# Kernel tuning notes

Hardware: AMD Instinct MI355X
Metric: run time of the kernel (lower is better)

## Reference

```python
import jax, jax.numpy as jnp
import numpy as np

POS_IOU, NEG_IOU = 0.5, 0.4
VAR = (0.1, 0.1, 0.2, 0.2)
ALPHA = 1.0
B, A, C, G = 16, 65536, 81, 32


def setup_inputs() -> dict:
    key = jax.random.key(0)
    k1, k2, k3, k4, k5, k6, k7 = jax.random.split(key, 7)
    cls_logits = jax.random.normal(k1, (B, A, C), dtype=jnp.float32)
    bbox_regs = jax.random.normal(k2, (B, A, 4), dtype=jnp.float32)
    # anchors: normalized cx,cy in (0,1), w,h positive
    anc_cxy = jax.random.uniform(k3, (A, 2), minval=0.05, maxval=0.95)
    anc_wh = jax.random.uniform(k4, (A, 2), minval=0.02, maxval=0.30)
    anchors_cxcywh = jnp.concatenate([anc_cxy, anc_wh], axis=-1).astype(jnp.float32)
    # GT boxes: valid normalized xyxy built from random cxcywh
    g_cxy = jax.random.uniform(k5, (B, G, 2), minval=0.1, maxval=0.9)
    g_wh = jax.random.uniform(k6, (B, G, 2), minval=0.05, maxval=0.40)
    x1y1 = jnp.clip(g_cxy - g_wh / 2, 0.0, 1.0)
    x2y2 = jnp.clip(g_cxy + g_wh / 2, 0.0, 1.0)
    gt_boxes = jnp.concatenate([x1y1, x2y2], axis=-1).astype(jnp.float32)
    gt_labels = jax.random.randint(k7, (B, G), 1, C).astype(jnp.int64)
    gt_valid = jnp.ones((B, G), dtype=bool)
    return {"cls_logits": cls_logits, "bbox_regs": bbox_regs,
            "anchors_cxcywh": anchors_cxcywh, "gt_boxes": gt_boxes,
            "gt_labels": gt_labels, "gt_valid": gt_valid}


def _encode(gt_xyxy, anc_cxcywh):
    # gt_xyxy [B,A,4], anc_cxcywh [A,4] -> offsets [B,A,4]
    x1, y1, x2, y2 = jnp.split(gt_xyxy, 4, axis=-1)
    gx, gy = (x1 + x2) / 2, (y1 + y2) / 2
    gw = jnp.clip(x2 - x1, 1e-6, None)
    gh = jnp.clip(y2 - y1, 1e-6, None)
    ax, ay, aw, ah = (anc_cxcywh[None, :, i:i + 1] for i in range(4))
    dx = (gx - ax) / (aw * VAR[0])
    dy = (gy - ay) / (ah * VAR[1])
    dw = jnp.log(gw / aw) / VAR[2]
    dh = jnp.log(gh / ah) / VAR[3]
    return jnp.concatenate([dx, dy, dw, dh], axis=-1)


def _forward(cls_logits, bbox_regs, anchors_cxcywh, gt_boxes, gt_labels, gt_valid):
    ax, ay, aw, ah = (anchors_cxcywh[:, i] for i in range(4))
    anc_xyxy = jnp.stack([ax - aw / 2, ay - ah / 2, ax + aw / 2, ay + ah / 2], axis=-1)  # [A,4]
    # IoU [B,A,G] (assignment is torch.no_grad in the original)
    tl = jnp.maximum(anc_xyxy[None, :, None, :2], gt_boxes[:, None, :, :2])
    br = jnp.minimum(anc_xyxy[None, :, None, 2:], gt_boxes[:, None, :, 2:])
    wh = jnp.clip(br - tl, 0.0, None)
    inter = wh[..., 0] * wh[..., 1]
    area_a = jnp.clip(anc_xyxy[:, 2] - anc_xyxy[:, 0], 0.0, None) * jnp.clip(anc_xyxy[:, 3] - anc_xyxy[:, 1], 0.0, None)
    area_b = jnp.clip(gt_boxes[..., 2] - gt_boxes[..., 0], 0.0, None) * jnp.clip(gt_boxes[..., 3] - gt_boxes[..., 1], 0.0, None)
    iou = inter / (area_a[None, :, None] + area_b[:, None, :] - inter + 1e-9)
    iou = jnp.where(gt_valid[:, None, :], iou, -1.0)  # padded GTs never match
    iou = jax.lax.stop_gradient(iou)

    iou_max = jnp.max(iou, axis=-1)              # [B,A]
    iou_idx = jnp.argmax(iou, axis=-1)           # [B,A]
    pos = iou_max >= POS_IOU
    ign = (iou_max > NEG_IOU) & ~pos

    matched_boxes = jnp.take_along_axis(gt_boxes, iou_idx[..., None], axis=1)   # [B,A,4]
    matched_labels = jnp.take_along_axis(gt_labels, iou_idx, axis=1)            # [B,A]
    cls_t = jnp.where(pos, matched_labels, jnp.where(ign, -1, 0))               # [B,A]
    reg_t = jax.lax.stop_gradient(_encode(matched_boxes, anchors_cxcywh))       # [B,A,4]

    # classification CE over valid (non-ignored) anchors, per-image mean
    logp = jax.nn.log_softmax(cls_logits, axis=-1)
    tgt = jnp.clip(cls_t, 0, None)
    ce = -jnp.take_along_axis(logp, tgt[..., None], axis=-1)[..., 0]            # [B,A]
    valid = cls_t >= 0
    n_valid = jnp.sum(valid, axis=1)
    cls_per = jnp.sum(ce * valid, axis=1) / jnp.maximum(n_valid, 1)
    total_cls = jnp.sum(jnp.where(n_valid > 0, cls_per, 0.0))

    # smooth L1 over positive anchors, per-image mean over pos*4 elements
    d = jnp.abs(bbox_regs - reg_t)
    sl1 = jnp.where(d < 1.0, 0.5 * d * d, d - 0.5)                              # [B,A,4]
    n_pos = jnp.sum(pos, axis=1)
    reg_per = jnp.sum(sl1 * pos[..., None], axis=(1, 2)) / jnp.maximum(4 * n_pos, 1)
    total_reg = jnp.sum(jnp.where(n_pos > 0, reg_per, 0.0))

    return total_cls + ALPHA * total_reg


def reference(cls_logits, bbox_regs, anchors_cxcywh, gt_boxes, gt_labels, gt_valid):
    return _forward(cls_logits, bbox_regs, anchors_cxcywh, gt_boxes, gt_labels, gt_valid)
```

## Files before the change

kernel.cpp:

```cpp
#include <hip/hip_runtime.h>
#include <math.h>

constexpr int kB = 16;
constexpr int kA = 65536;
constexpr int kC = 81;
constexpr int kG = 32;
constexpr int kBlockA = 256;
constexpr int kBlocksPerB = kA / kBlockA;
constexpr float kPosIou = 0.5f;
constexpr float kNegIou = 0.4f;

struct F5 { float4 x0, x1, x2, x3, x4; };

__device__ __forceinline__ float4 ldf4(const float* p) {
    float4 v; __builtin_memcpy(&v, p, 16); return v;
}
__device__ __forceinline__ F5 load5(const float* row, int q) {
    const float* r = row + (q << 2);
    F5 f;
    f.x0 = ldf4(r);
    f.x1 = ldf4(r + 16);
    f.x2 = ldf4(r + 32);
    f.x3 = ldf4(r + 48);
    f.x4 = ldf4(r + 64);
    return f;
}
__device__ __forceinline__ float sumexp(const F5& f) {
    float s0 = __expf(f.x0.x) + __expf(f.x0.y) + __expf(f.x0.z) + __expf(f.x0.w);
    float s1 = __expf(f.x1.x) + __expf(f.x1.y) + __expf(f.x1.z) + __expf(f.x1.w);
    float s2 = __expf(f.x2.x) + __expf(f.x2.y) + __expf(f.x2.z) + __expf(f.x2.w);
    float s3 = __expf(f.x3.x) + __expf(f.x3.y) + __expf(f.x3.z) + __expf(f.x3.w);
    float s4 = __expf(f.x4.x) + __expf(f.x4.y) + __expf(f.x4.z) + __expf(f.x4.w);
    return ((s0 + s1) + (s2 + s3)) + s4;
}

__global__ __launch_bounds__(256) void ssd_main_kernel(
    const float* __restrict__ cls_logits,
    const float* __restrict__ bbox_regs,
    const float* __restrict__ anchors,
    const float* __restrict__ gt_boxes,
    const int*   __restrict__ gt_labels,
    const int*   __restrict__ gt_valid,
    float* __restrict__ ws)
{
    __shared__ float s_gx1[kG], s_gy1[kG], s_gx2[kG], s_gy2[kG], s_area[kG];
    __shared__ int   s_lab[kG], s_val[kG];
    __shared__ int   s_t[kBlockA];
    __shared__ float s_tv[kBlockA];
    __shared__ float s_e80[kBlockA];
    __shared__ float s_red[4][4];

    const int tid = threadIdx.x;
    const int b  = blockIdx.x / kBlocksPerB;
    const int a0 = (blockIdx.x % kBlocksPerB) * kBlockA;

    if (tid < kG) {
        float4 gb = *reinterpret_cast<const float4*>(gt_boxes + ((size_t)b * kG + tid) * 4);
        s_gx1[tid] = gb.x; s_gy1[tid] = gb.y; s_gx2[tid] = gb.z; s_gy2[tid] = gb.w;
        s_area[tid] = fmaxf(gb.z - gb.x, 0.f) * fmaxf(gb.w - gb.y, 0.f);
        s_lab[tid] = gt_labels[b * kG + tid];
        s_val[tid] = gt_valid[b * kG + tid];
    }
    __syncthreads();

    const int wave = tid >> 6;
    const int lane = tid & 63;
    const int g4   = lane >> 2;
    const int q    = lane & 3;
    const float* row0 = cls_logits + ((size_t)b * kA + a0 + 0 * 64 + wave * 16 + g4) * kC;
    const float* row1 = cls_logits + ((size_t)b * kA + a0 + 1 * 64 + wave * 16 + g4) * kC;
    const float* row2 = cls_logits + ((size_t)b * kA + a0 + 2 * 64 + wave * 16 + g4) * kC;
    const float* row3 = cls_logits + ((size_t)b * kA + a0 + 3 * 64 + wave * 16 + g4) * kC;
    F5 va = load5(row0, q);
    F5 vb = load5(row1, q);

    const int a = a0 + tid;
    float4 anc = *reinterpret_cast<const float4*>(anchors + (size_t)a * 4);
    const float ax1 = anc.x - anc.z * 0.5f, ay1 = anc.y - anc.w * 0.5f;
    const float ax2 = anc.x + anc.z * 0.5f, ay2 = anc.y + anc.w * 0.5f;
    const float area_a = fmaxf(ax2 - ax1, 0.f) * fmaxf(ay2 - ay1, 0.f);

    float best = -2.0f;
    int   bidx = 0;
    #pragma unroll 8
    for (int g = 0; g < kG; ++g) {
        float tlx = fmaxf(ax1, s_gx1[g]);
        float tly = fmaxf(ay1, s_gy1[g]);
        float brx = fminf(ax2, s_gx2[g]);
        float bry = fminf(ay2, s_gy2[g]);
        float w = fmaxf(brx - tlx, 0.f);
        float h = fmaxf(bry - tly, 0.f);
        float inter = w * h;
        float iou = __fdividef(inter, area_a + s_area[g] - inter + 1e-9f);
        iou = s_val[g] ? iou : -1.0f;
        if (iou > best) { best = iou; bidx = g; }
    }
    const bool pos = best >= kPosIou;
    const bool ign = (best > kNegIou) && !pos;
    const int cls_t = pos ? s_lab[bidx] : (ign ? -1 : 0);
    s_t[tid] = cls_t;

    const float* own = cls_logits + ((size_t)b * kA + a0 + tid) * kC;
    s_tv[tid]  = own[cls_t < 0 ? 0 : cls_t];
    s_e80[tid] = own[80];

    float reg_sum = 0.f;
    if (pos) {
        float gx1 = s_gx1[bidx], gy1 = s_gy1[bidx], gx2 = s_gx2[bidx], gy2 = s_gy2[bidx];
        float gx = (gx1 + gx2) * 0.5f, gy = (gy1 + gy2) * 0.5f;
        float gw = fmaxf(gx2 - gx1, 1e-6f), gh = fmaxf(gy2 - gy1, 1e-6f);
        float dx = __fdividef(gx - anc.x, anc.z * 0.1f);
        float dy = __fdividef(gy - anc.y, anc.w * 0.1f);
        float dw = __logf(__fdividef(gw, anc.z)) * 5.0f;
        float dh = __logf(__fdividef(gh, anc.w)) * 5.0f;
        float4 br = *reinterpret_cast<const float4*>(bbox_regs + ((size_t)b * kA + a) * 4);
        float d0 = fabsf(br.x - dx), d1 = fabsf(br.y - dy);
        float d2 = fabsf(br.z - dw), d3 = fabsf(br.w - dh);
        reg_sum = (d0 < 1.f ? 0.5f * d0 * d0 : d0 - 0.5f)
                + (d1 < 1.f ? 0.5f * d1 * d1 : d1 - 0.5f)
                + (d2 < 1.f ? 0.5f * d2 * d2 : d2 - 0.5f)
                + (d3 < 1.f ? 0.5f * d3 * d3 : d3 - 0.5f);
    }
    __syncthreads();

    int   ct0 = 0, ct1 = 0, ct2 = 0, ct3 = 0;
    float tv0 = 0.f, tv1 = 0.f, tv2 = 0.f, tv3 = 0.f;
    float e80_0 = 0.f, e80_1 = 0.f, e80_2 = 0.f, e80_3 = 0.f;
    if (q == 0) {
        const int r0 = 0 * 64 + wave * 16 + g4;
        const int r1 = 1 * 64 + wave * 16 + g4;
        const int r2 = 2 * 64 + wave * 16 + g4;
        const int r3 = 3 * 64 + wave * 16 + g4;
        ct0 = s_t[r0]; tv0 = s_tv[r0]; e80_0 = s_e80[r0];
        ct1 = s_t[r1]; tv1 = s_tv[r1]; e80_1 = s_e80[r1];
        ct2 = s_t[r2]; tv2 = s_tv[r2]; e80_2 = s_e80[r2];
        ct3 = s_t[r3]; tv3 = s_tv[r3]; e80_3 = s_e80[r3];
    }

    float ce_acc = 0.f;
    {
        float S = sumexp(va);
        if (q == 0) S += __expf(e80_0);
        S += __shfl_xor(S, 1);
        S += __shfl_xor(S, 2);
        if (q == 0 && ct0 >= 0) ce_acc += __logf(S) - tv0;
    }
    va = load5(row2, q);
    {
        float S = sumexp(vb);
        if (q == 0) S += __expf(e80_1);
        S += __shfl_xor(S, 1);
        S += __shfl_xor(S, 2);
        if (q == 0 && ct1 >= 0) ce_acc += __logf(S) - tv1;
    }
    vb = load5(row3, q);
    {
        float S = sumexp(va);
        if (q == 0) S += __expf(e80_2);
        S += __shfl_xor(S, 1);
        S += __shfl_xor(S, 2);
        if (q == 0 && ct2 >= 0) ce_acc += __logf(S) - tv2;
    }
    {
        float S = sumexp(vb);
        if (q == 0) S += __expf(e80_3);
        S += __shfl_xor(S, 1);
        S += __shfl_xor(S, 2);
        if (q == 0 && ct3 >= 0) ce_acc += __logf(S) - tv3;
    }

    float v0 = ce_acc;
    float v1 = (cls_t >= 0) ? 1.f : 0.f;
    float v2 = reg_sum;
    float v3 = pos ? 1.f : 0.f;
    #pragma unroll
    for (int off = 32; off > 0; off >>= 1) {
        v0 += __shfl_xor(v0, off);
        v1 += __shfl_xor(v1, off);
        v2 += __shfl_xor(v2, off);
        v3 += __shfl_xor(v3, off);
    }
    if (lane == 0) {
        s_red[wave][0] = v0; s_red[wave][1] = v1;
        s_red[wave][2] = v2; s_red[wave][3] = v3;
    }
    __syncthreads();
    if (tid < 4) {
        float acc = s_red[0][tid] + s_red[1][tid] + s_red[2][tid] + s_red[3][tid];
        ws[(size_t)blockIdx.x * 4 + tid] = acc;
    }
}

__global__ __launch_bounds__(256) void ssd_final_kernel(
    const float* __restrict__ ws, float* __restrict__ out)
{
    __shared__ float s_per_b[kB];
    const int tid = threadIdx.x;
    const int b = tid >> 4;
    const int i = tid & 15;
    float a0 = 0.f, a1 = 0.f, a2 = 0.f, a3 = 0.f;
    #pragma unroll
    for (int k = 0; k < 16; ++k) {
        const float4 v = *reinterpret_cast<const float4*>(
            ws + ((size_t)((b << 8) + (k << 4) + i)) * 4);
        a0 += v.x; a1 += v.y; a2 += v.z; a3 += v.w;
    }
    #pragma unroll
    for (int off = 1; off < 16; off <<= 1) {
        a0 += __shfl_xor(a0, off);
        a1 += __shfl_xor(a1, off);
        a2 += __shfl_xor(a2, off);
        a3 += __shfl_xor(a3, off);
    }
    if (i == 0) {
        float cls = (a1 > 0.f) ? a0 / fmaxf(a1, 1.f) : 0.f;
        float reg = (a3 > 0.f) ? a2 / fmaxf(4.f * a3, 1.f) : 0.f;
        s_per_b[b] = cls + reg;
    }
    __syncthreads();
    if (tid == 0) {
        float t = 0.f;
        #pragma unroll
        for (int x = 0; x < kB; ++x) t += s_per_b[x];
        out[0] = t;
    }
}

extern "C" void kernel_launch(void* const* d_in, const int* in_sizes, int n_in,
                              void* d_out, int out_size, void* d_ws, size_t ws_size,
                              hipStream_t stream) {
    const float* cls_logits = (const float*)d_in[0];
    const float* bbox_regs  = (const float*)d_in[1];
    const float* anchors    = (const float*)d_in[2];
    const float* gt_boxes   = (const float*)d_in[3];
    const int*   gt_labels  = (const int*)d_in[4];
    const int*   gt_valid   = (const int*)d_in[5];
    float* ws  = (float*)d_ws;
    float* out = (float*)d_out;

    ssd_main_kernel<<<dim3(kB * kBlocksPerB), dim3(kBlockA), 0, stream>>>(
        cls_logits, bbox_regs, anchors, gt_boxes, gt_labels, gt_valid, ws);
    ssd_final_kernel<<<dim3(1), dim3(kBlockA), 0, stream>>>(ws, out);
}
```

Measured before the change: 72.86 us.

## Shuffle targets within waves, pick target logit from registers, fuse final reduction

Remaps logit rows so each wave processes the same anchors it assigned, letting targets move via cross-lane shuffles instead of shared memory and a block barrier. The target logit is selected from already-loaded registers, removing scattered per-anchor global loads. The separate finalize kernel is replaced by per-image atomic accumulation and a last-block counter, which needs a memset each call and relies on atomic ordering without an explicit fence.

```diff
diff --git a/kernel.cpp b/kernel.cpp
--- a/kernel.cpp
+++ b/kernel.cpp
@@ -7,6 +7,7 @@
 constexpr int kG = 32;
 constexpr int kBlockA = 256;
 constexpr int kBlocksPerB = kA / kBlockA;
+constexpr int kGrid = kB * kBlocksPerB;
 constexpr float kPosIou = 0.5f;
 constexpr float kNegIou = 0.4f;
 
@@ -33,6 +34,16 @@
     float s4 = __expf(f.x4.x) + __expf(f.x4.y) + __expf(f.x4.z) + __expf(f.x4.w);
     return ((s0 + s1) + (s2 + s3)) + s4;
 }
+__device__ __forceinline__ float pick_t(const F5& f, int te, int q, float e80) {
+    if (te >= 80) return (q == 0) ? e80 : 0.f;
+    const int k_t = te >> 4;
+    const int q_t = (te >> 2) & 3;
+    const int e_t = te & 3;
+    if (q != q_t) return 0.f;
+    float4 c = (k_t == 0) ? f.x0 : (k_t == 1) ? f.x1 : (k_t == 2) ? f.x2
+             : (k_t == 3) ? f.x3 : f.x4;
+    return (e_t == 0) ? c.x : (e_t == 1) ? c.y : (e_t == 2) ? c.z : c.w;
+}
 
 __global__ __launch_bounds__(256) void ssd_main_kernel(
     const float* __restrict__ cls_logits,
@@ -41,14 +52,14 @@
     const float* __restrict__ gt_boxes,
     const int*   __restrict__ gt_labels,
     const int*   __restrict__ gt_valid,
-    float* __restrict__ ws)
+    float* __restrict__ ws,
+    int*   __restrict__ counter,
+    float* __restrict__ out)
 {
     __shared__ float s_gx1[kG], s_gy1[kG], s_gx2[kG], s_gy2[kG], s_area[kG];
     __shared__ int   s_lab[kG], s_val[kG];
-    __shared__ int   s_t[kBlockA];
-    __shared__ float s_tv[kBlockA];
-    __shared__ float s_e80[kBlockA];
     __shared__ float s_red[4][4];
+    __shared__ int   s_last;
 
     const int tid = threadIdx.x;
     const int b  = blockIdx.x / kBlocksPerB;
@@ -67,12 +78,15 @@
     const int lane = tid & 63;
     const int g4   = lane >> 2;
     const int q    = lane & 3;
-    const float* row0 = cls_logits + ((size_t)b * kA + a0 + 0 * 64 + wave * 16 + g4) * kC;
-    const float* row1 = cls_logits + ((size_t)b * kA + a0 + 1 * 64 + wave * 16 + g4) * kC;
-    const float* row2 = cls_logits + ((size_t)b * kA + a0 + 2 * 64 + wave * 16 + g4) * kC;
-    const float* row3 = cls_logits + ((size_t)b * kA + a0 + 3 * 64 + wave * 16 + g4) * kC;
+    const float* wrow = cls_logits + ((size_t)b * kA + a0 + wave * 64) * kC;
+    const float* row0 = wrow + (size_t)(0 * 16 + g4) * kC;
+    const float* row1 = wrow + (size_t)(1 * 16 + g4) * kC;
+    const float* row2 = wrow + (size_t)(2 * 16 + g4) * kC;
+    const float* row3 = wrow + (size_t)(3 * 16 + g4) * kC;
     F5 va = load5(row0, q);
     F5 vb = load5(row1, q);
+    float e80_0 = 0.f, e80_1 = 0.f, e80_2 = 0.f, e80_3 = 0.f;
+    if (q == 0) { e80_0 = row0[80]; e80_1 = row1[80]; e80_2 = row2[80]; e80_3 = row3[80]; }
 
     const int a = a0 + tid;
     float4 anc = *reinterpret_cast<const float4*>(anchors + (size_t)a * 4);
@@ -98,11 +112,6 @@
     const bool pos = best >= kPosIou;
     const bool ign = (best > kNegIou) && !pos;
     const int cls_t = pos ? s_lab[bidx] : (ign ? -1 : 0);
-    s_t[tid] = cls_t;
-
-    const float* own = cls_logits + ((size_t)b * kA + a0 + tid) * kC;
-    s_tv[tid]  = own[cls_t < 0 ? 0 : cls_t];
-    s_e80[tid] = own[80];
 
     float reg_sum = 0.f;
     if (pos) {
@@ -121,52 +130,50 @@
                 + (d2 < 1.f ? 0.5f * d2 * d2 : d2 - 0.5f)
                 + (d3 < 1.f ? 0.5f * d3 * d3 : d3 - 0.5f);
     }
-    __syncthreads();
-
-    int   ct0 = 0, ct1 = 0, ct2 = 0, ct3 = 0;
-    float tv0 = 0.f, tv1 = 0.f, tv2 = 0.f, tv3 = 0.f;
-    float e80_0 = 0.f, e80_1 = 0.f, e80_2 = 0.f, e80_3 = 0.f;
-    if (q == 0) {
-        const int r0 = 0 * 64 + wave * 16 + g4;
-        const int r1 = 1 * 64 + wave * 16 + g4;
-        const int r2 = 2 * 64 + wave * 16 + g4;
-        const int r3 = 3 * 64 + wave * 16 + g4;
-        ct0 = s_t[r0]; tv0 = s_tv[r0]; e80_0 = s_e80[r0];
-        ct1 = s_t[r1]; tv1 = s_tv[r1]; e80_1 = s_e80[r1];
-        ct2 = s_t[r2]; tv2 = s_tv[r2]; e80_2 = s_e80[r2];
-        ct3 = s_t[r3]; tv3 = s_tv[r3]; e80_3 = s_e80[r3];
-    }
+
+    const int ct0 = __shfl(cls_t, 0 * 16 + g4);
+    const int ct1 = __shfl(cls_t, 1 * 16 + g4);
+    const int ct2 = __shfl(cls_t, 2 * 16 + g4);
+    const int ct3 = __shfl(cls_t, 3 * 16 + g4);
 
     float ce_acc = 0.f;
     {
+        const int te = ct0 < 0 ? 0 : ct0;
         float S = sumexp(va);
         if (q == 0) S += __expf(e80_0);
-        S += __shfl_xor(S, 1);
-        S += __shfl_xor(S, 2);
-        if (q == 0 && ct0 >= 0) ce_acc += __logf(S) - tv0;
+        float T = pick_t(va, te, q, e80_0);
+        S += __shfl_xor(S, 1);  T += __shfl_xor(T, 1);
+        S += __shfl_xor(S, 2);  T += __shfl_xor(T, 2);
+        if (q == 0 && ct0 >= 0) ce_acc += __logf(S) - T;
     }
     va = load5(row2, q);
     {
+        const int te = ct1 < 0 ? 0 : ct1;
         float S = sumexp(vb);
         if (q == 0) S += __expf(e80_1);
-        S += __shfl_xor(S, 1);
-        S += __shfl_xor(S, 2);
-        if (q == 0 && ct1 >= 0) ce_acc += __logf(S) - tv1;
+        float T = pick_t(vb, te, q, e80_1);
+        S += __shfl_xor(S, 1);  T += __shfl_xor(T, 1);
+        S += __shfl_xor(S, 2);  T += __shfl_xor(T, 2);
+        if (q == 0 && ct1 >= 0) ce_acc += __logf(S) - T;
     }
     vb = load5(row3, q);
     {
+        const int te = ct2 < 0 ? 0 : ct2;
         float S = sumexp(va);
         if (q == 0) S += __expf(e80_2);
-        S += __shfl_xor(S, 1);
-        S += __shfl_xor(S, 2);
-        if (q == 0 && ct2 >= 0) ce_acc += __logf(S) - tv2;
-    }
-    {
+        float T = pick_t(va, te, q, e80_2);
+        S += __shfl_xor(S, 1);  T += __shfl_xor(T, 1);
+        S += __shfl_xor(S, 2);  T += __shfl_xor(T, 2);
+        if (q == 0 && ct2 >= 0) ce_acc += __logf(S) - T;
+    }
+    {
+        const int te = ct3 < 0 ? 0 : ct3;
         float S = sumexp(vb);
         if (q == 0) S += __expf(e80_3);
-        S += __shfl_xor(S, 1);
-        S += __shfl_xor(S, 2);
-        if (q == 0 && ct3 >= 0) ce_acc += __logf(S) - tv3;
+        float T = pick_t(vb, te, q, e80_3);
+        S += __shfl_xor(S, 1);  T += __shfl_xor(T, 1);
+        S += __shfl_xor(S, 2);  T += __shfl_xor(T, 2);
+        if (q == 0 && ct3 >= 0) ce_acc += __logf(S) - T;
     }
 
     float v0 = ce_acc;
@@ -187,42 +194,24 @@
     __syncthreads();
     if (tid < 4) {
         float acc = s_red[0][tid] + s_red[1][tid] + s_red[2][tid] + s_red[3][tid];
-        ws[(size_t)blockIdx.x * 4 + tid] = acc;
-    }
-}
-
-__global__ __launch_bounds__(256) void ssd_final_kernel(
-    const float* __restrict__ ws, float* __restrict__ out)
-{
-    __shared__ float s_per_b[kB];
-    const int tid = threadIdx.x;
-    const int b = tid >> 4;
-    const int i = tid & 15;
-    float a0 = 0.f, a1 = 0.f, a2 = 0.f, a3 = 0.f;
-    #pragma unroll
-    for (int k = 0; k < 16; ++k) {
-        const float4 v = *reinterpret_cast<const float4*>(
-            ws + ((size_t)((b << 8) + (k << 4) + i)) * 4);
-        a0 += v.x; a1 += v.y; a2 += v.z; a3 += v.w;
-    }
-    #pragma unroll
-    for (int off = 1; off < 16; off <<= 1) {
-        a0 += __shfl_xor(a0, off);
-        a1 += __shfl_xor(a1, off);
-        a2 += __shfl_xor(a2, off);
-        a3 += __shfl_xor(a3, off);
-    }
-    if (i == 0) {
-        float cls = (a1 > 0.f) ? a0 / fmaxf(a1, 1.f) : 0.f;
-        float reg = (a3 > 0.f) ? a2 / fmaxf(4.f * a3, 1.f) : 0.f;
-        s_per_b[b] = cls + reg;
-    }
-    __syncthreads();
-    if (tid == 0) {
-        float t = 0.f;
+        atomicAdd(&ws[b * 4 + tid], acc);
+    }
+    __syncthreads();
+    if (tid == 0)
+        s_last = (atomicAdd(counter, 1) == kGrid - 1);
+    __syncthreads();
+    if (s_last && tid < kB) {
+        float sce  = atomicAdd(&ws[tid * 4 + 0], 0.f);
+        float nval = atomicAdd(&ws[tid * 4 + 1], 0.f);
+        float ssl  = atomicAdd(&ws[tid * 4 + 2], 0.f);
+        float npos = atomicAdd(&ws[tid * 4 + 3], 0.f);
+        float cls = (nval > 0.f) ? sce / fmaxf(nval, 1.f) : 0.f;
+        float reg = (npos > 0.f) ? ssl / fmaxf(4.f * npos, 1.f) : 0.f;
+        float v = cls + reg;
         #pragma unroll
-        for (int x = 0; x < kB; ++x) t += s_per_b[x];
-        out[0] = t;
+        for (int off = 1; off < kB; off <<= 1)
+            v += __shfl_xor(v, off);
+        if (tid == 0) out[0] = v;
     }
 }
 
@@ -235,10 +224,13 @@
     const float* gt_boxes   = (const float*)d_in[3];
     const int*   gt_labels  = (const int*)d_in[4];
     const int*   gt_valid   = (const int*)d_in[5];
-    float* ws  = (float*)d_ws;
-    float* out = (float*)d_out;
-
-    ssd_main_kernel<<<dim3(kB * kBlocksPerB), dim3(kBlockA), 0, stream>>>(
-        cls_logits, bbox_regs, anchors, gt_boxes, gt_labels, gt_valid, ws);
-    ssd_final_kernel<<<dim3(1), dim3(kBlockA), 0, stream>>>(ws, out);
-}
+    float* ws      = (float*)d_ws;
+    int*   counter = (int*)((char*)d_ws + 256);
+    float* out     = (float*)d_out;
+
+    hipMemsetAsync(d_ws, 0, 260, stream);
+
+    ssd_main_kernel<<<dim3(kGrid), dim3(kBlockA), 0, stream>>>(
+        cls_logits, bbox_regs, anchors, gt_boxes, gt_labels, gt_valid,
+        ws, counter, out);
+}
```

New measurement: 137.9 us. +89.2%, slower.

## Split anchor assignment and cross-entropy into separate kernels with int8 targets

Applied to the files above, without the earlier changes.

Anchor matching and the smooth-L1 term move into their own kernel, which writes per-anchor class targets as int8 to the workspace. A second kernel streams the logits, 512 rows per block, with software-prefetched double buffering. It takes the target logit from the registers already loaded instead of issuing scattered per-row loads. This removes the serial dependency of the logit stream on the IoU loop and the uncoalesced target gather, at the cost of an extra launch and a small int8 round trip. The fused path remains as a fallback when the workspace is too small.

```diff
diff --git a/kernel.cpp b/kernel.cpp
--- a/kernel.cpp
+++ b/kernel.cpp
@@ -5,8 +5,6 @@
 constexpr int kA = 65536;
 constexpr int kC = 81;
 constexpr int kG = 32;
-constexpr int kBlockA = 256;
-constexpr int kBlocksPerB = kA / kBlockA;
 constexpr float kPosIou = 0.5f;
 constexpr float kNegIou = 0.4f;
 
@@ -33,26 +31,43 @@
     float s4 = __expf(f.x4.x) + __expf(f.x4.y) + __expf(f.x4.z) + __expf(f.x4.w);
     return ((s0 + s1) + (s2 + s3)) + s4;
 }
-
-__global__ __launch_bounds__(256) void ssd_main_kernel(
-    const float* __restrict__ cls_logits,
+__device__ __forceinline__ float pick_t(const F5& f, int te, int q, float e80) {
+    if (te >= 80) return (q == 0) ? e80 : 0.f;
+    const int k_t = te >> 4;
+    const int q_t = (te >> 2) & 3;
+    const int e_t = te & 3;
+    if (q != q_t) return 0.f;
+    float4 c = (k_t == 0) ? f.x0 : (k_t == 1) ? f.x1 : (k_t == 2) ? f.x2
+             : (k_t == 3) ? f.x3 : f.x4;
+    return (e_t == 0) ? c.x : (e_t == 1) ? c.y : (e_t == 2) ? c.z : c.w;
+}
+
+constexpr size_t kOffT8  = 0;
+constexpr size_t kOffAsg = (size_t)kB * kA;
+constexpr size_t kOffCe  = kOffAsg + (size_t)4096 * 4 * 4;
+constexpr size_t kWsNeed = kOffCe + (size_t)2048 * 4;
+
+constexpr int kAsgBlkA   = 256;
+constexpr int kAsgPerB   = kA / kAsgBlkA;
+constexpr int kRowsPerCe = 512;
+constexpr int kCePerB    = kA / kRowsPerCe;
+
+__global__ __launch_bounds__(256) void ssd_assign_kernel(
     const float* __restrict__ bbox_regs,
     const float* __restrict__ anchors,
     const float* __restrict__ gt_boxes,
     const int*   __restrict__ gt_labels,
     const int*   __restrict__ gt_valid,
-    float* __restrict__ ws)
+    signed char* __restrict__ cls_t8,
+    float* __restrict__ wsa)
 {
     __shared__ float s_gx1[kG], s_gy1[kG], s_gx2[kG], s_gy2[kG], s_area[kG];
     __shared__ int   s_lab[kG], s_val[kG];
-    __shared__ int   s_t[kBlockA];
-    __shared__ float s_tv[kBlockA];
-    __shared__ float s_e80[kBlockA];
     __shared__ float s_red[4][4];
 
     const int tid = threadIdx.x;
-    const int b  = blockIdx.x / kBlocksPerB;
-    const int a0 = (blockIdx.x % kBlocksPerB) * kBlockA;
+    const int b  = blockIdx.x / kAsgPerB;
+    const int a0 = (blockIdx.x % kAsgPerB) * kAsgBlkA;
 
     if (tid < kG) {
         float4 gb = *reinterpret_cast<const float4*>(gt_boxes + ((size_t)b * kG + tid) * 4);
@@ -62,17 +77,6 @@
         s_val[tid] = gt_valid[b * kG + tid];
     }
     __syncthreads();
-
-    const int wave = tid >> 6;
-    const int lane = tid & 63;
-    const int g4   = lane >> 2;
-    const int q    = lane & 3;
-    const float* row0 = cls_logits + ((size_t)b * kA + a0 + 0 * 64 + wave * 16 + g4) * kC;
-    const float* row1 = cls_logits + ((size_t)b * kA + a0 + 1 * 64 + wave * 16 + g4) * kC;
-    const float* row2 = cls_logits + ((size_t)b * kA + a0 + 2 * 64 + wave * 16 + g4) * kC;
-    const float* row3 = cls_logits + ((size_t)b * kA + a0 + 3 * 64 + wave * 16 + g4) * kC;
-    F5 va = load5(row0, q);
-    F5 vb = load5(row1, q);
 
     const int a = a0 + tid;
     float4 anc = *reinterpret_cast<const float4*>(anchors + (size_t)a * 4);
@@ -98,11 +102,7 @@
     const bool pos = best >= kPosIou;
     const bool ign = (best > kNegIou) && !pos;
     const int cls_t = pos ? s_lab[bidx] : (ign ? -1 : 0);
-    s_t[tid] = cls_t;
-
-    const float* own = cls_logits + ((size_t)b * kA + a0 + tid) * kC;
-    s_tv[tid]  = own[cls_t < 0 ? 0 : cls_t];
-    s_e80[tid] = own[80];
+    cls_t8[(size_t)b * kA + a] = (signed char)cls_t;
 
     float reg_sum = 0.f;
     if (pos) {
@@ -121,6 +121,230 @@
                 + (d2 < 1.f ? 0.5f * d2 * d2 : d2 - 0.5f)
                 + (d3 < 1.f ? 0.5f * d3 * d3 : d3 - 0.5f);
     }
+
+    const int wave = tid >> 6;
+    const int lane = tid & 63;
+    float v1 = (cls_t >= 0) ? 1.f : 0.f;
+    float v2 = reg_sum;
+    float v3 = pos ? 1.f : 0.f;
+    #pragma unroll
+    for (int off = 32; off > 0; off >>= 1) {
+        v1 += __shfl_xor(v1, off);
+        v2 += __shfl_xor(v2, off);
+        v3 += __shfl_xor(v3, off);
+    }
+    if (lane == 0) {
+        s_red[wave][0] = 0.f; s_red[wave][1] = v1;
+        s_red[wave][2] = v2;  s_red[wave][3] = v3;
+    }
+    __syncthreads();
+    if (tid < 4) {
+        float acc = s_red[0][tid] + s_red[1][tid] + s_red[2][tid] + s_red[3][tid];
+        wsa[(size_t)blockIdx.x * 4 + tid] = acc;
+    }
+}
+
+__global__ __launch_bounds__(256) void ssd_ce_kernel(
+    const float* __restrict__ cls_logits,
+    const signed char* __restrict__ cls_t8,
+    float* __restrict__ wsce)
+{
+    __shared__ float s_red[4];
+    const int tid  = threadIdx.x;
+    const int wave = tid >> 6;
+    const int lane = tid & 63;
+    const int g4   = lane >> 2;
+    const int q    = lane & 3;
+    const int blk   = blockIdx.x;
+    const int b     = blk / kCePerB;
+    const int chunk = blk % kCePerB;
+
+    const size_t rbase = (size_t)b * kA + chunk * kRowsPerCe + wave * 16 + g4;
+    const float* rp = cls_logits + rbase * kC;
+    const signed char* ctp = cls_t8 + rbase;
+    const size_t kIt = (size_t)64 * kC;
+
+    F5 va = load5(rp, q);
+    F5 vb = load5(rp + kIt, q);
+    int cta = ctp[0];
+    int ctb = ctp[64];
+    float ea = 0.f, eb = 0.f;
+    if (q == 0) { ea = rp[80]; eb = rp[kIt + 80]; }
+
+    float ce = 0.f;
+    #pragma unroll
+    for (int it = 0; it < 8; it += 2) {
+        {
+            float S = sumexp(va);
+            float T = pick_t(va, cta < 0 ? 0 : cta, q, ea);
+            const bool vld = (cta >= 0);
+            const float ecur = ea;
+            if (it + 2 < 8) {
+                va = load5(rp + (it + 2) * kIt, q);
+                cta = ctp[(it + 2) * 64];
+                if (q == 0) ea = rp[(it + 2) * kIt + 80];
+            }
+            if (q == 0) S += __expf(ecur);
+            S += __shfl_xor(S, 1);  T += __shfl_xor(T, 1);
+            S += __shfl_xor(S, 2);  T += __shfl_xor(T, 2);
+            if (q == 0 && vld) ce += __logf(S) - T;
+        }
+        {
+            float S = sumexp(vb);
+            float T = pick_t(vb, ctb < 0 ? 0 : ctb, q, eb);
+            const bool vld = (ctb >= 0);
+            const float ecur = eb;
+            if (it + 3 < 8) {
+                vb = load5(rp + (it + 3) * kIt, q);
+                ctb = ctp[(it + 3) * 64];
+                if (q == 0) eb = rp[(it + 3) * kIt + 80];
+            }
+            if (q == 0) S += __expf(ecur);
+            S += __shfl_xor(S, 1);  T += __shfl_xor(T, 1);
+            S += __shfl_xor(S, 2);  T += __shfl_xor(T, 2);
+            if (q == 0 && vld) ce += __logf(S) - T;
+        }
+    }
+
+    #pragma unroll
+    for (int off = 32; off > 0; off >>= 1)
+        ce += __shfl_xor(ce, off);
+    if (lane == 0) s_red[wave] = ce;
+    __syncthreads();
+    if (tid == 0)
+        wsce[blk] = s_red[0] + s_red[1] + s_red[2] + s_red[3];
+}
+
+__global__ __launch_bounds__(256) void ssd_final_split(
+    const float* __restrict__ wsa,
+    const float* __restrict__ wsce,
+    float* __restrict__ out)
+{
+    __shared__ float s_per_b[kB];
+    const int tid = threadIdx.x;
+    const int b = tid >> 4;
+    const int i = tid & 15;
+    float a0 = 0.f, a1 = 0.f, a2 = 0.f, a3 = 0.f;
+    #pragma unroll
+    for (int k = 0; k < 16; ++k) {
+        const float4 v = *reinterpret_cast<const float4*>(
+            wsa + ((size_t)(b * 256 + k * 16 + i)) * 4);
+        a1 += v.y; a2 += v.z; a3 += v.w;
+    }
+    #pragma unroll
+    for (int k = 0; k < 8; ++k)
+        a0 += wsce[b * 128 + k * 16 + i];
+    #pragma unroll
+    for (int off = 1; off < 16; off <<= 1) {
+        a0 += __shfl_xor(a0, off);
+        a1 += __shfl_xor(a1, off);
+        a2 += __shfl_xor(a2, off);
+        a3 += __shfl_xor(a3, off);
+    }
+    if (i == 0) {
+        float cls = (a1 > 0.f) ? a0 / fmaxf(a1, 1.f) : 0.f;
+        float reg = (a3 > 0.f) ? a2 / fmaxf(4.f * a3, 1.f) : 0.f;
+        s_per_b[b] = cls + reg;
+    }
+    __syncthreads();
+    if (tid == 0) {
+        float t = 0.f;
+        #pragma unroll
+        for (int x = 0; x < kB; ++x) t += s_per_b[x];
+        out[0] = t;
+    }
+}
+
+constexpr int kFBlkA   = 256;
+constexpr int kFPerB   = kA / kFBlkA;
+
+__global__ __launch_bounds__(256) void ssd_fused_kernel(
+    const float* __restrict__ cls_logits,
+    const float* __restrict__ bbox_regs,
+    const float* __restrict__ anchors,
+    const float* __restrict__ gt_boxes,
+    const int*   __restrict__ gt_labels,
+    const int*   __restrict__ gt_valid,
+    float* __restrict__ ws)
+{
+    __shared__ float s_gx1[kG], s_gy1[kG], s_gx2[kG], s_gy2[kG], s_area[kG];
+    __shared__ int   s_lab[kG], s_val[kG];
+    __shared__ int   s_t[kFBlkA];
+    __shared__ float s_tv[kFBlkA];
+    __shared__ float s_e80[kFBlkA];
+    __shared__ float s_red[4][4];
+
+    const int tid = threadIdx.x;
+    const int b  = blockIdx.x / kFPerB;
+    const int a0 = (blockIdx.x % kFPerB) * kFBlkA;
+
+    if (tid < kG) {
+        float4 gb = *reinterpret_cast<const float4*>(gt_boxes + ((size_t)b * kG + tid) * 4);
+        s_gx1[tid] = gb.x; s_gy1[tid] = gb.y; s_gx2[tid] = gb.z; s_gy2[tid] = gb.w;
+        s_area[tid] = fmaxf(gb.z - gb.x, 0.f) * fmaxf(gb.w - gb.y, 0.f);
+        s_lab[tid] = gt_labels[b * kG + tid];
+        s_val[tid] = gt_valid[b * kG + tid];
+    }
+    __syncthreads();
+
+    const int wave = tid >> 6;
+    const int lane = tid & 63;
+    const int g4   = lane >> 2;
+    const int q    = lane & 3;
+    const float* row0 = cls_logits + ((size_t)b * kA + a0 + 0 * 64 + wave * 16 + g4) * kC;
+    const float* row1 = cls_logits + ((size_t)b * kA + a0 + 1 * 64 + wave * 16 + g4) * kC;
+    const float* row2 = cls_logits + ((size_t)b * kA + a0 + 2 * 64 + wave * 16 + g4) * kC;
+    const float* row3 = cls_logits + ((size_t)b * kA + a0 + 3 * 64 + wave * 16 + g4) * kC;
+    F5 va = load5(row0, q);
+    F5 vb = load5(row1, q);
+
+    const int a = a0 + tid;
+    float4 anc = *reinterpret_cast<const float4*>(anchors + (size_t)a * 4);
+    const float ax1 = anc.x - anc.z * 0.5f, ay1 = anc.y - anc.w * 0.5f;
+    const float ax2 = anc.x + anc.z * 0.5f, ay2 = anc.y + anc.w * 0.5f;
+    const float area_a = fmaxf(ax2 - ax1, 0.f) * fmaxf(ay2 - ay1, 0.f);
+
+    float best = -2.0f;
+    int   bidx = 0;
+    #pragma unroll 8
+    for (int g = 0; g < kG; ++g) {
+        float tlx = fmaxf(ax1, s_gx1[g]);
+        float tly = fmaxf(ay1, s_gy1[g]);
+        float brx = fminf(ax2, s_gx2[g]);
+        float bry = fminf(ay2, s_gy2[g]);
+        float w = fmaxf(brx - tlx, 0.f);
+        float h = fmaxf(bry - tly, 0.f);
+        float inter = w * h;
+        float iou = __fdividef(inter, area_a + s_area[g] - inter + 1e-9f);
+        iou = s_val[g] ? iou : -1.0f;
+        if (iou > best) { best = iou; bidx = g; }
+    }
+    const bool pos = best >= kPosIou;
+    const bool ign = (best > kNegIou) && !pos;
+    const int cls_t = pos ? s_lab[bidx] : (ign ? -1 : 0);
+    s_t[tid] = cls_t;
+
+    const float* own = cls_logits + ((size_t)b * kA + a0 + tid) * kC;
+    s_tv[tid]  = own[cls_t < 0 ? 0 : cls_t];
+    s_e80[tid] = own[80];
+
+    float reg_sum = 0.f;
+    if (pos) {
+        float gx1 = s_gx1[bidx], gy1 = s_gy1[bidx], gx2 = s_gx2[bidx], gy2 = s_gy2[bidx];
+        float gx = (gx1 + gx2) * 0.5f, gy = (gy1 + gy2) * 0.5f;
+        float gw = fmaxf(gx2 - gx1, 1e-6f), gh = fmaxf(gy2 - gy1, 1e-6f);
+        float dx = __fdividef(gx - anc.x, anc.z * 0.1f);
+        float dy = __fdividef(gy - anc.y, anc.w * 0.1f);
+        float dw = __logf(__fdividef(gw, anc.z)) * 5.0f;
+        float dh = __logf(__fdividef(gh, anc.w)) * 5.0f;
+        float4 br = *reinterpret_cast<const float4*>(bbox_regs + ((size_t)b * kA + a) * 4);
+        float d0 = fabsf(br.x - dx), d1 = fabsf(br.y - dy);
+        float d2 = fabsf(br.z - dw), d3 = fabsf(br.w - dh);
+        reg_sum = (d0 < 1.f ? 0.5f * d0 * d0 : d0 - 0.5f)
+                + (d1 < 1.f ? 0.5f * d1 * d1 : d1 - 0.5f)
+                + (d2 < 1.f ? 0.5f * d2 * d2 : d2 - 0.5f)
+                + (d3 < 1.f ? 0.5f * d3 * d3 : d3 - 0.5f);
+    }
     __syncthreads();
 
     int   ct0 = 0, ct1 = 0, ct2 = 0, ct3 = 0;
@@ -138,31 +362,27 @@
     }
 
     float ce_acc = 0.f;
-    {
-        float S = sumexp(va);
+    {   float S = sumexp(va);
         if (q == 0) S += __expf(e80_0);
         S += __shfl_xor(S, 1);
         S += __shfl_xor(S, 2);
         if (q == 0 && ct0 >= 0) ce_acc += __logf(S) - tv0;
     }
     va = load5(row2, q);
-    {
-        float S = sumexp(vb);
+    {   float S = sumexp(vb);
         if (q == 0) S += __expf(e80_1);
         S += __shfl_xor(S, 1);
         S += __shfl_xor(S, 2);
         if (q == 0 && ct1 >= 0) ce_acc += __logf(S) - tv1;
     }
     vb = load5(row3, q);
-    {
-        float S = sumexp(va);
+    {   float S = sumexp(va);
         if (q == 0) S += __expf(e80_2);
         S += __shfl_xor(S, 1);
         S += __shfl_xor(S, 2);
         if (q == 0 && ct2 >= 0) ce_acc += __logf(S) - tv2;
     }
-    {
-        float S = sumexp(vb);
+    {   float S = sumexp(vb);
         if (q == 0) S += __expf(e80_3);
         S += __shfl_xor(S, 1);
         S += __shfl_xor(S, 2);
@@ -191,7 +411,7 @@
     }
 }
 
-__global__ __launch_bounds__(256) void ssd_final_kernel(
+__global__ __launch_bounds__(256) void ssd_final_fused(
     const float* __restrict__ ws, float* __restrict__ out)
 {
     __shared__ float s_per_b[kB];
@@ -235,10 +455,21 @@
     const float* gt_boxes   = (const float*)d_in[3];
     const int*   gt_labels  = (const int*)d_in[4];
     const int*   gt_valid   = (const int*)d_in[5];
-    float* ws  = (float*)d_ws;
     float* out = (float*)d_out;
 
-    ssd_main_kernel<<<dim3(kB * kBlocksPerB), dim3(kBlockA), 0, stream>>>(
-        cls_logits, bbox_regs, anchors, gt_boxes, gt_labels, gt_valid, ws);
-    ssd_final_kernel<<<dim3(1), dim3(kBlockA), 0, stream>>>(ws, out);
-}
+    if (ws_size >= kWsNeed) {
+        signed char* cls_t8 = (signed char*)d_ws + kOffT8;
+        float* wsa  = (float*)((char*)d_ws + kOffAsg);
+        float* wsce = (float*)((char*)d_ws + kOffCe);
+        ssd_assign_kernel<<<dim3(kB * kAsgPerB), dim3(256), 0, stream>>>(
+            bbox_regs, anchors, gt_boxes, gt_labels, gt_valid, cls_t8, wsa);
+        ssd_ce_kernel<<<dim3(kB * kCePerB), dim3(256), 0, stream>>>(
+            cls_logits, cls_t8, wsce);
+        ssd_final_split<<<dim3(1), dim3(256), 0, stream>>>(wsa, wsce, out);
+    } else {
+        float* ws = (float*)d_ws;
+        ssd_fused_kernel<<<dim3(kB * kFPerB), dim3(kFBlkA), 0, stream>>>(
+            cls_logits, bbox_regs, anchors, gt_boxes, gt_labels, gt_valid, ws);
+        ssd_final_fused<<<dim3(1), dim3(256), 0, stream>>>(ws, out);
+    }
+}
```

New measurement: 152.3 us. 109% more time.

## Compute log-sum-exp before anchor matching and exchange logS through shared memory

Applied to the files above, without the earlier changes.

Reorders the kernel so each 4-lane group computes the log-sum-exp of its logit rows first and writes logS per anchor to shared memory. The IoU matching and target gather then run after a single barrier, with each thread combining its own logS with its target logit. This drops the separate target, target-value and last-logit shared arrays, one barrier, and the extra last-column loads. The risk is that the matching ALU work no longer hides the logit load latency, and the target-logit gather now happens after the bulk stream.

```diff
diff --git a/kernel.cpp b/kernel.cpp
--- a/kernel.cpp
+++ b/kernel.cpp
@@ -45,9 +45,7 @@
 {
     __shared__ float s_gx1[kG], s_gy1[kG], s_gx2[kG], s_gy2[kG], s_area[kG];
     __shared__ int   s_lab[kG], s_val[kG];
-    __shared__ int   s_t[kBlockA];
-    __shared__ float s_tv[kBlockA];
-    __shared__ float s_e80[kBlockA];
+    __shared__ float s_logS[kBlockA];
     __shared__ float s_red[4][4];
 
     const int tid = threadIdx.x;
@@ -61,21 +59,56 @@
         s_lab[tid] = gt_labels[b * kG + tid];
         s_val[tid] = gt_valid[b * kG + tid];
     }
-    __syncthreads();
+    const int a = a0 + tid;
+    float4 anc = *reinterpret_cast<const float4*>(anchors + (size_t)a * 4);
 
     const int wave = tid >> 6;
     const int lane = tid & 63;
     const int g4   = lane >> 2;
     const int q    = lane & 3;
-    const float* row0 = cls_logits + ((size_t)b * kA + a0 + 0 * 64 + wave * 16 + g4) * kC;
-    const float* row1 = cls_logits + ((size_t)b * kA + a0 + 1 * 64 + wave * 16 + g4) * kC;
-    const float* row2 = cls_logits + ((size_t)b * kA + a0 + 2 * 64 + wave * 16 + g4) * kC;
-    const float* row3 = cls_logits + ((size_t)b * kA + a0 + 3 * 64 + wave * 16 + g4) * kC;
-    F5 va = load5(row0, q);
-    F5 vb = load5(row1, q);
-
-    const int a = a0 + tid;
-    float4 anc = *reinterpret_cast<const float4*>(anchors + (size_t)a * 4);
+    const size_t kIt = (size_t)64 * kC;
+    const float* rp = cls_logits + ((size_t)b * kA + a0 + wave * 16 + g4) * kC;
+
+    F5 va = load5(rp, q);
+    F5 vb = load5(rp + kIt, q);
+    float ea = 0.f, eb = 0.f;
+    if (q == 0) { ea = rp[80]; eb = rp[kIt + 80]; }
+
+    {
+        float S = sumexp(va);
+        if (q == 0) S += __expf(ea);
+        va = load5(rp + 2 * kIt, q);
+        if (q == 0) ea = rp[2 * kIt + 80];
+        S += __shfl_xor(S, 1);
+        S += __shfl_xor(S, 2);
+        if (q == 0) s_logS[0 * 64 + wave * 16 + g4] = __logf(S);
+    }
+    {
+        float S = sumexp(vb);
+        if (q == 0) S += __expf(eb);
+        vb = load5(rp + 3 * kIt, q);
+        if (q == 0) eb = rp[3 * kIt + 80];
+        S += __shfl_xor(S, 1);
+        S += __shfl_xor(S, 2);
+        if (q == 0) s_logS[1 * 64 + wave * 16 + g4] = __logf(S);
+    }
+    {
+        float S = sumexp(va);
+        if (q == 0) S += __expf(ea);
+        S += __shfl_xor(S, 1);
+        S += __shfl_xor(S, 2);
+        if (q == 0) s_logS[2 * 64 + wave * 16 + g4] = __logf(S);
+    }
+    {
+        float S = sumexp(vb);
+        if (q == 0) S += __expf(eb);
+        S += __shfl_xor(S, 1);
+        S += __shfl_xor(S, 2);
+        if (q == 0) s_logS[3 * 64 + wave * 16 + g4] = __logf(S);
+    }
+
+    __syncthreads();
+
     const float ax1 = anc.x - anc.z * 0.5f, ay1 = anc.y - anc.w * 0.5f;
     const float ax2 = anc.x + anc.z * 0.5f, ay2 = anc.y + anc.w * 0.5f;
     const float area_a = fmaxf(ax2 - ax1, 0.f) * fmaxf(ay2 - ay1, 0.f);
@@ -98,11 +131,10 @@
     const bool pos = best >= kPosIou;
     const bool ign = (best > kNegIou) && !pos;
     const int cls_t = pos ? s_lab[bidx] : (ign ? -1 : 0);
-    s_t[tid] = cls_t;
 
     const float* own = cls_logits + ((size_t)b * kA + a0 + tid) * kC;
-    s_tv[tid]  = own[cls_t < 0 ? 0 : cls_t];
-    s_e80[tid] = own[80];
+    const float tv = own[cls_t < 0 ? 0 : cls_t];
+    const float ce_acc = (cls_t >= 0) ? (s_logS[tid] - tv) : 0.f;
 
     float reg_sum = 0.f;
     if (pos) {
@@ -121,53 +153,6 @@
                 + (d2 < 1.f ? 0.5f * d2 * d2 : d2 - 0.5f)
                 + (d3 < 1.f ? 0.5f * d3 * d3 : d3 - 0.5f);
     }
-    __syncthreads();
-
-    int   ct0 = 0, ct1 = 0, ct2 = 0, ct3 = 0;
-    float tv0 = 0.f, tv1 = 0.f, tv2 = 0.f, tv3 = 0.f;
-    float e80_0 = 0.f, e80_1 = 0.f, e80_2 = 0.f, e80_3 = 0.f;
-    if (q == 0) {
-        const int r0 = 0 * 64 + wave * 16 + g4;
-        const int r1 = 1 * 64 + wave * 16 + g4;
-        const int r2 = 2 * 64 + wave * 16 + g4;
-        const int r3 = 3 * 64 + wave * 16 + g4;
-        ct0 = s_t[r0]; tv0 = s_tv[r0]; e80_0 = s_e80[r0];
-        ct1 = s_t[r1]; tv1 = s_tv[r1]; e80_1 = s_e80[r1];
-        ct2 = s_t[r2]; tv2 = s_tv[r2]; e80_2 = s_e80[r2];
-        ct3 = s_t[r3]; tv3 = s_tv[r3]; e80_3 = s_e80[r3];
-    }
-
-    float ce_acc = 0.f;
-    {
-        float S = sumexp(va);
-        if (q == 0) S += __expf(e80_0);
-        S += __shfl_xor(S, 1);
-        S += __shfl_xor(S, 2);
-        if (q == 0 && ct0 >= 0) ce_acc += __logf(S) - tv0;
-    }
-    va = load5(row2, q);
-    {
-        float S = sumexp(vb);
-        if (q == 0) S += __expf(e80_1);
-        S += __shfl_xor(S, 1);
-        S += __shfl_xor(S, 2);
-        if (q == 0 && ct1 >= 0) ce_acc += __logf(S) - tv1;
-    }
-    vb = load5(row3, q);
-    {
-        float S = sumexp(va);
-        if (q == 0) S += __expf(e80_2);
-        S += __shfl_xor(S, 1);
-        S += __shfl_xor(S, 2);
-        if (q == 0 && ct2 >= 0) ce_acc += __logf(S) - tv2;
-    }
-    {
-        float S = sumexp(vb);
-        if (q == 0) S += __expf(e80_3);
-        S += __shfl_xor(S, 1);
-        S += __shfl_xor(S, 2);
-        if (q == 0 && ct3 >= 0) ce_acc += __logf(S) - tv3;
-    }
 
     float v0 = ce_acc;
     float v1 = (cls_t >= 0) ? 1.f : 0.f;
```

After: 75.64 us. +3.8%, slower.
